# Kernel optimization log

Measured on AMD Instinct MI355X. Metric: run time of the kernel, lower is better.

The kernel has to match this reference:

```python
import jax, jax.numpy as jnp
import numpy as np

G = 8192          # graphs in batch
A = 5             # num_agents (nodes per graph)
N = G * A         # total nodes
IN_CH = 29
HID = 64
HEADS = 8
D = HID * HEADS   # 512, node/graph feature dim
NOPT = 4
ADIM = 3


def _lin(key, fan_in, fan_out):
    return jax.random.normal(key, (fan_in, fan_out), jnp.float32) / np.sqrt(fan_in)


def setup_inputs() -> dict:
    key = jax.random.key(0)
    ks = jax.random.split(key, 40)
    # --- graph structure: G fully-connected 5-node graphs + self loops ---
    pairs = np.array([(i, j) for i in range(A) for j in range(A) if i != j])  # [20,2]
    base = (np.arange(G)[:, None] * A)
    src = (base + pairs[None, :, 0]).reshape(-1)
    dst = (base + pairs[None, :, 1]).reshape(-1)
    # GATConv adds self loops (fill_value=0.0 for edge_attr)
    loop = np.arange(N)
    edge_src = jnp.asarray(np.concatenate([src, loop]), jnp.int32)
    edge_dst = jnp.asarray(np.concatenate([dst, loop]), jnp.int32)
    e_real = jax.random.uniform(ks[0], (src.shape[0], 1), jnp.float32)
    edge_attr = jnp.concatenate([e_real, jnp.zeros((N, 1), jnp.float32)], axis=0)
    batch_map = jnp.asarray(np.repeat(np.arange(G), A), jnp.int32)
    x = jax.random.normal(ks[1], (N, IN_CH), jnp.float32)
    sc = 1.0 / np.sqrt(HID)
    inp = dict(
        x=x, edge_attr=edge_attr, edge_src=edge_src, edge_dst=edge_dst, batch_map=batch_map,
        # conv1
        W1=_lin(ks[2], IN_CH, D), as1=jax.random.normal(ks[3], (HEADS, HID)) * sc,
        ad1=jax.random.normal(ks[4], (HEADS, HID)) * sc, We1=_lin(ks[5], 1, D),
        ae1=jax.random.normal(ks[6], (HEADS, HID)) * sc, b1=jnp.zeros((D,), jnp.float32),
        # conv2
        W2=_lin(ks[7], D, D), as2=jax.random.normal(ks[8], (HEADS, HID)) * sc,
        ad2=jax.random.normal(ks[9], (HEADS, HID)) * sc, We2=_lin(ks[10], 1, D),
        ae2=jax.random.normal(ks[11], (HEADS, HID)) * sc, b2=jnp.zeros((D,), jnp.float32),
        # policy-over-options head
        pw1=_lin(ks[12], D, 2 * HID), pb1=jnp.zeros((2 * HID,)), pw2=_lin(ks[13], 2 * HID, NOPT), pb2=jnp.zeros((NOPT,)),
        # q-options head
        qw1=_lin(ks[14], D, 2 * HID), qb1=jnp.zeros((2 * HID,)), qw2=_lin(ks[15], 2 * HID, NOPT), qb2=jnp.zeros((NOPT,)),
        # intra-option actor head (option 0), input dim = node + graph feature = 2*D
        aw1=_lin(ks[16], 2 * D, 2 * HID), ab1=jnp.zeros((2 * HID,)), aw2=_lin(ks[17], 2 * HID, 2 * ADIM), ab2=jnp.zeros((2 * ADIM,)),
        # termination head (option 0)
        tw1=_lin(ks[18], D, HID), tb1=jnp.zeros((HID,)), tw2=_lin(ks[19], HID, 1), tb2=jnp.zeros((1,)),
        action_limits=jnp.array([1.0, 1.0, 3.14159], jnp.float32),
    )
    return inp


def _gat(x, src, dst, eattr, W, a_s, a_d, We, a_e, b):
    n = x.shape[0]
    h = (x @ W).reshape(n, HEADS, HID)                      # [N,H,C]
    e = (eattr @ We).reshape(-1, HEADS, HID)                # [E,H,C]
    lg = ((h * a_s).sum(-1)[src] + (h * a_d).sum(-1)[dst]
          + (e * a_e).sum(-1))                              # [E,H]
    lg = jnp.where(lg > 0, lg, 0.2 * lg)                    # leaky_relu(0.2)
    m = jax.ops.segment_max(lg, dst, num_segments=n)
    p = jnp.exp(lg - m[dst])
    denom = jax.ops.segment_sum(p, dst, num_segments=n)[dst] + 1e-16
    alpha = p / denom                                       # scatter-softmax over dst
    out = jax.ops.segment_sum(alpha[:, :, None] * h[src], dst, num_segments=n)
    return out.reshape(n, HEADS * HID) + b


def reference(x, edge_attr, edge_src, edge_dst, batch_map,
              W1, as1, ad1, We1, ae1, b1,
              W2, as2, ad2, We2, ae2, b2,
              pw1, pb1, pw2, pb2, qw1, qb1, qw2, qb2,
              aw1, ab1, aw2, ab2, tw1, tb1, tw2, tb2, action_limits):
    h = jax.nn.relu(_gat(x, edge_src, edge_dst, edge_attr, W1, as1, ad1, We1, ae1, b1))
    h = jax.nn.relu(_gat(h, edge_src, edge_dst, edge_attr, W2, as2, ad2, We2, ae2, b2))
    # global_mean_pool
    cnt = jax.ops.segment_sum(jnp.ones((h.shape[0],), h.dtype), batch_map, num_segments=G)
    g = jax.ops.segment_sum(h, batch_map, num_segments=G) / cnt[:, None]   # [G,D]
    pi = jax.nn.relu(g @ pw1 + pb1) @ pw2 + pb2                            # [G,NOPT]
    q = jax.nn.relu(g @ qw1 + qb1) @ qw2 + qb2                             # [G,NOPT]
    term = jax.nn.sigmoid(jax.nn.relu(g @ tw1 + tb1) @ tw2 + tb2)          # [G,1]
    # per-graph first num_agents nodes == all nodes here (5 per graph)
    agent = h.reshape(G, A, D)
    comb = jnp.concatenate([agent, jnp.broadcast_to(g[:, None, :], (G, A, D))], axis=-1)
    ho = jax.nn.relu(comb @ aw1 + ab1) @ aw2 + ab2                          # [G,A,6]
    mean_raw, log_std_raw = jnp.split(ho, 2, axis=-1)
    mean = jnp.tanh(mean_raw) * action_limits                               # [G,A,3]
    std = 0.05 + jax.nn.sigmoid(log_std_raw) * 0.45 + 1e-6
    return jnp.concatenate([pi, q, term, mean.reshape(G, -1), std.reshape(G, -1)], axis=1)
```

## Files before the change

### kernel.cpp

```cpp
#include <hip/hip_runtime.h>
#include <hip/hip_bf16.h>
#include <math.h>

#define GG 8192
#define AA 5
#define NN (GG * AA)
#define DD 512

typedef unsigned short ushort_t;
typedef unsigned int uint_t;

__device__ inline float bf2f(ushort_t u) {
  union { uint_t i; float f; } c; c.i = ((uint_t)u) << 16; return c.f;
}
__device__ inline ushort_t f2bf(float f) {
  union { float f; uint_t i; } c; c.f = f;
  uint_t r = c.i + 0x7fffu + ((c.i >> 16) & 1u);
  return (ushort_t)(r >> 16);
}

using frag8 = __attribute__((ext_vector_type(8))) short;
using f32x4 = __attribute__((ext_vector_type(4))) float;

typedef __attribute__((address_space(3))) void lds_void;
typedef __attribute__((address_space(1))) const void gbl_void;
#define GLL(g, l) __builtin_amdgcn_global_load_lds((gbl_void*)(g), (lds_void*)(l), 16, 0, 0)

__device__ inline int xcd_swz(int bid, int nwg) {
  return (bid & 7) * (nwg >> 3) + (bid >> 3);
}

__global__ __launch_bounds__(256) void k_prep(
    const float* __restrict__ x, const float* __restrict__ W1,
    const float* __restrict__ W2, const float* __restrict__ pw1,
    const float* __restrict__ qw1, const float* __restrict__ tw1,
    const float* __restrict__ aw1, const float* __restrict__ pb1,
    const float* __restrict__ qb1, const float* __restrict__ tb1,
    const float* __restrict__ ab1, const float* __restrict__ We1,
    const float* __restrict__ ae1, const float* __restrict__ We2,
    const float* __restrict__ ae2, const float* __restrict__ as1,
    const float* __restrict__ ad1, const float* __restrict__ as2,
    const float* __restrict__ ad2, const float* __restrict__ pw2,
    const float* __restrict__ pb2, const float* __restrict__ qw2,
    const float* __restrict__ qb2, const float* __restrict__ tw2,
    const float* __restrict__ tb2, const float* __restrict__ aw2,
    const float* __restrict__ ab2, ushort_t* __restrict__ xpad32,
    ushort_t* __restrict__ W1T32, ushort_t* __restrict__ W2T,
    ushort_t* __restrict__ WcatT, ushort_t* __restrict__ aw1topT,
    ushort_t* __restrict__ wsc1T, ushort_t* __restrict__ wsc2T,
    float* __restrict__ bcat, float* __restrict__ sce,
    float* __restrict__ woutT, float* __restrict__ bout) {
  int b = blockIdx.x;
  int t = threadIdx.x;
  if (b < 1024) {
    int i = b * 256 + t;
    int n = i >> 9, k = i & 511;
    W2T[(size_t)n * 512 + k] = f2bf(W2[(size_t)k * 512 + n]);
    float v;
    if (n < 128)      v = pw1[(size_t)k * 128 + n];
    else if (n < 256) v = qw1[(size_t)k * 128 + (n - 128)];
    else if (n < 320) v = tw1[(size_t)k * 64 + (n - 256)];
    else if (n < 448) v = aw1[(size_t)(512 + k) * 128 + (n - 320)];
    else              v = 0.f;
    WcatT[(size_t)n * 512 + k] = f2bf(v);
    if (n < 128) aw1topT[(size_t)n * 512 + k] = f2bf(aw1[(size_t)k * 128 + n]);
    if (k == 0) {
      float bv;
      if (n < 128)      bv = pb1[n];
      else if (n < 256) bv = qb1[n - 128];
      else if (n < 320) bv = tb1[n - 256];
      else if (n < 448) bv = ab1[n - 320];
      else              bv = 0.f;
      bcat[n] = bv;
    }
    if (i < 512 * 32) {
      int nn = i >> 5, kk = i & 31;
      W1T32[i] = (kk < 29) ? f2bf(W1[(size_t)kk * 512 + nn]) : (ushort_t)0;
    }
    if (i < 8192) {
      int k2 = i & 511, s = i >> 9;
      int head = s >> 1;
      const float* av = ((s & 1) ? ad2 : as2) + head * 64;
      const float* wr = W2 + (size_t)k2 * 512 + head * 64;
      float val = 0.f;
      for (int c = 0; c < 64; ++c) val = fmaf(wr[c], av[c], val);
      wsc2T[i] = f2bf(val);
    }
    if (i < 512) {
      int k1 = i & 31, s = i >> 5;
      int head = s >> 1;
      float val = 0.f;
      if (k1 < 29) {
        const float* av = ((s & 1) ? ad1 : as1) + head * 64;
        const float* wr = W1 + (size_t)k1 * 512 + head * 64;
        for (int c = 0; c < 64; ++c) val = fmaf(wr[c], av[c], val);
      }
      wsc1T[i] = f2bf(val);
    }
    if (i < 16) {
      int h = i & 7;
      const float* Wp = (i < 8) ? We1 : We2;
      const float* ap = (i < 8) ? ae1 : ae2;
      float c = 0.f;
      for (int k2 = 0; k2 < 64; ++k2) c = fmaf(Wp[h * 64 + k2], ap[h * 64 + k2], c);
      sce[i] = c;
    }
    if (i < 5120) {
      int j = i / 40, o = i % 40;
      float wv;
      if (o < 4)       wv = pw2[j * 4 + o];
      else if (o < 8)  wv = qw2[j * 4 + (o - 4)];
      else if (o == 8) wv = (j < 64) ? tw2[j] : 0.f;
      else if (o < 24) wv = aw2[j * 6 + (o - 9) % 3];
      else if (o < 39) wv = aw2[j * 6 + 3 + (o - 24) % 3];
      else             wv = 0.f;
      woutT[i] = wv;
      if (j == 0) {
        float bv;
        if (o < 4)       bv = pb2[o];
        else if (o < 8)  bv = qb2[o - 4];
        else if (o == 8) bv = tb2[0];
        else if (o < 24) bv = ab2[(o - 9) % 3];
        else if (o < 39) bv = ab2[3 + (o - 24) % 3];
        else             bv = 0.f;
        bout[o] = bv;
      }
    }
  } else {
    int i = (b - 1024) * 256 + t;
    int n = i >> 5, k = i & 31;
    xpad32[i] = (k < 29) ? f2bf(x[(size_t)n * 29 + k]) : (ushort_t)0;
  }
}

__global__ __launch_bounds__(1024) void k_mega(
    const ushort_t* __restrict__ xpad32, const ushort_t* __restrict__ W1T32,
    const ushort_t* __restrict__ wsc1T, const ushort_t* __restrict__ W2T,
    const ushort_t* __restrict__ wsc2T, const float* __restrict__ eattr,
    const float* __restrict__ sce, const float* __restrict__ b1,
    const float* __restrict__ b2, ushort_t* __restrict__ h2,
    ushort_t* __restrict__ gmean) {
  __shared__ __align__(16) char smem[149504];
  const int t = threadIdx.x;
  const int lane = t & 63;
  const int w = t >> 6;
  const int l15 = lane & 15;
  const int ko2 = ((((lane >> 4) ^ (lane & 3) ^ ((lane >> 2) & 3)) & 3) * 16);
  int lid = xcd_swz(blockIdx.x, gridDim.x);
  const int m0 = lid * 80;
  const int g0 = lid * 16;
  ushort_t* h1buf = (ushort_t*)smem;
  float* sal = (float*)(smem + 124160);
  float* sss = (float*)(smem + 136960);
  float* ssd = (float*)(smem + 139520);
  const f32x4 zz = {0.f, 0.f, 0.f, 0.f};
  f32x4 acc[5][2], asc[5];
#pragma unroll
  for (int mt = 0; mt < 5; ++mt) { acc[mt][0] = zz; acc[mt][1] = zz; asc[mt] = zz; }

  {
#pragma unroll
    for (int r_ = 0; r_ < 2; ++r_) {
      int c_ = t + r_ * 1024; int row_ = c_ >> 2;
      int sw_ = ((((c_ & 3) ^ (row_ & 3) ^ ((row_ >> 2) & 3)) & 3)) * 8;
      GLL(W1T32 + (size_t)row_ * 32 + sw_, smem + 81920 + c_ * 16);
    }
    if (t < 320) {
      int c_ = t; int row_ = c_ >> 2;
      int sw_ = ((((c_ & 3) ^ (row_ & 3) ^ ((row_ >> 2) & 3)) & 3)) * 8;
      GLL(xpad32 + (size_t)(m0 + row_) * 32 + sw_, smem + 114688 + c_ * 16);
    } else if (t < 384) {
      int c_ = t - 320; int row_ = c_ >> 2;
      int sw_ = ((((c_ & 3) ^ (row_ & 3) ^ ((row_ >> 2) & 3)) & 3)) * 8;
      GLL(wsc1T + (size_t)row_ * 32 + sw_, smem + 119808 + c_ * 16);
    }
  }
  asm volatile("s_waitcnt vmcnt(0)" ::: "memory");
  __builtin_amdgcn_s_barrier();
  {
    const char* bb = smem + 81920;
    const char* aa = smem + 114688;
    const char* sb = smem + 119808;
    frag8 af[5], bfr[2];
#pragma unroll
    for (int mt = 0; mt < 5; ++mt)
      af[mt] = *(const frag8*)(aa + (mt * 16 + l15) * 64 + ko2);
#pragma unroll
    for (int n = 0; n < 2; ++n)
      bfr[n] = *(const frag8*)(bb + ((2 * w + n) * 16 + l15) * 64 + ko2);
#pragma unroll
    for (int mt = 0; mt < 5; ++mt)
#pragma unroll
      for (int n = 0; n < 2; ++n)
        acc[mt][n] = __builtin_amdgcn_mfma_f32_16x16x32_bf16(af[mt], bfr[n], acc[mt][n], 0, 0, 0);
    if (w == 15) {
      frag8 sfr = *(const frag8*)(sb + l15 * 64 + ko2);
#pragma unroll
      for (int mt = 0; mt < 5; ++mt)
        asc[mt] = __builtin_amdgcn_mfma_f32_16x16x32_bf16(af[mt], sfr, asc[mt], 0, 0, 0);
    }
  }
  if (w == 15) {
    float* dst = (l15 & 1) ? ssd : sss;
    int hd = l15 >> 1;
    int q4 = (lane >> 4) * 4;
#pragma unroll
    for (int mt = 0; mt < 5; ++mt)
#pragma unroll
      for (int r = 0; r < 4; ++r)
        dst[(mt * 16 + q4 + r) * 8 + hd] = asc[mt][r];
  }
  __syncthreads();
  if (t < 640) {
    int gi = t / 40, jh = t % 40;
    int j = jh >> 3, hd = jh & 7;
    int g = g0 + gi;
    float sdj = ssd[(gi * 5 + j) * 8 + hd];
    float ce = sce[hd];
    float lg[5], mx = -1e30f;
#pragma unroll
    for (int i = 0; i < 5; ++i) {
      float l = sss[(gi * 5 + i) * 8 + hd] + sdj;
      if (i != j) l = fmaf(eattr[(size_t)g * 20 + i * 4 + (j > i ? j - 1 : j)], ce, l);
      l = l > 0.f ? l : 0.2f * l;
      lg[i] = l; mx = fmaxf(mx, l);
    }
    float s = 0.f;
#pragma unroll
    for (int i = 0; i < 5; ++i) { lg[i] = __expf(lg[i] - mx); s += lg[i]; }
    float inv = 1.f / (s + 1e-16f);
#pragma unroll
    for (int i = 0; i < 5; ++i) sal[((gi * 5 + j) * 5 + i) * 8 + hd] = lg[i] * inv;
  }
  __syncthreads();
  {
    float* hbf = (float*)(smem + 81920);
#pragma unroll
    for (int p = 0; p < 4; ++p) {
      if ((w >> 2) == p) {
        int q4 = (lane >> 4) * 4;
#pragma unroll
        for (int mt = 0; mt < 5; ++mt)
#pragma unroll
          for (int n = 0; n < 2; ++n) {
            int lc = (w & 3) * 32 + n * 16 + l15;
#pragma unroll
            for (int r = 0; r < 4; ++r)
              hbf[(mt * 16 + q4 + r) * 132 + lc] = acc[mt][n][r];
          }
      }
      __syncthreads();
      if (t < 512) {
        int gi = t >> 5, cq = t & 31;
        int hd = 2 * p + (cq >> 4);
        int cg = p * 128 + cq * 4;
        float hv[5][4];
#pragma unroll
        for (int i = 0; i < 5; ++i)
          *(float4*)hv[i] = *(const float4*)&hbf[(gi * 5 + i) * 132 + cq * 4];
        float4 bb4 = *(const float4*)&b1[cg];
        int chunk = cg >> 5, slot = (cg >> 3) & 3, boff = (cg & 7) * 2;
#pragma unroll
        for (int j = 0; j < 5; ++j) {
          float o0 = bb4.x, o1 = bb4.y, o2 = bb4.z, o3 = bb4.w;
#pragma unroll
          for (int i = 0; i < 5; ++i) {
            float a = sal[((gi * 5 + j) * 5 + i) * 8 + hd];
            o0 = fmaf(a, hv[i][0], o0); o1 = fmaf(a, hv[i][1], o1);
            o2 = fmaf(a, hv[i][2], o2); o3 = fmaf(a, hv[i][3], o3);
          }
          o0 = fmaxf(o0, 0.f); o1 = fmaxf(o1, 0.f);
          o2 = fmaxf(o2, 0.f); o3 = fmaxf(o3, 0.f);
          uint2 wv_;
          wv_.x = (uint_t)f2bf(o0) | ((uint_t)f2bf(o1) << 16);
          wv_.y = (uint_t)f2bf(o2) | ((uint_t)f2bf(o3) << 16);
          int row = gi * 5 + j;
          int phys = slot ^ (row & 3) ^ ((row >> 2) & 3);
          *(uint2*)((char*)h1buf + chunk * 5120 + row * 64 + phys * 16 + boff) = wv_;
        }
      }
      __syncthreads();
    }
  }

#pragma unroll
  for (int mt = 0; mt < 5; ++mt) { acc[mt][0] = zz; acc[mt][1] = zz; asc[mt] = zz; }
#define FS2(bi, kk0)                                                           \
  {                                                                            \
    char* bb_ = smem + 81920 + (bi) * 32768;                                   \
    char* sb_ = smem + 147456 + (bi) * 1024;                                   \
    _Pragma("unroll")                                                          \
    for (int r_ = 0; r_ < 2; ++r_) {                                           \
      int c_ = t + r_ * 1024; int row_ = c_ >> 2;                              \
      int sw_ = ((((c_ & 3) ^ (row_ & 3) ^ ((row_ >> 2) & 3)) & 3)) * 8;       \
      GLL(W2T + (size_t)row_ * 512 + (kk0) + sw_, bb_ + c_ * 16);              \
    }                                                                          \
    if (t < 64) {                                                              \
      int c_ = t; int row_ = c_ >> 2;                                          \
      int sw_ = ((((c_ & 3) ^ (row_ & 3) ^ ((row_ >> 2) & 3)) & 3)) * 8;       \
      GLL(wsc2T + (size_t)row_ * 512 + (kk0) + sw_, sb_ + c_ * 16);            \
    }                                                                          \
  }
  FS2(0, 0);
  asm volatile("s_waitcnt vmcnt(0)" ::: "memory");
  __builtin_amdgcn_s_barrier();
  for (int ts = 0; ts < 16; ++ts) {
    int cur = ts & 1;
    if (ts + 1 < 16) FS2(cur ^ 1, (ts + 1) * 32);
    const char* bb = smem + 81920 + cur * 32768;
    const char* aa = (const char*)h1buf + ts * 5120;
    const char* sb = smem + 147456 + cur * 1024;
    frag8 af[5], bfr[2];
#pragma unroll
    for (int mt = 0; mt < 5; ++mt)
      af[mt] = *(const frag8*)(aa + (mt * 16 + l15) * 64 + ko2);
#pragma unroll
    for (int n = 0; n < 2; ++n)
      bfr[n] = *(const frag8*)(bb + ((2 * w + n) * 16 + l15) * 64 + ko2);
    __builtin_amdgcn_s_setprio(1);
#pragma unroll
    for (int mt = 0; mt < 5; ++mt)
#pragma unroll
      for (int n = 0; n < 2; ++n)
        acc[mt][n] = __builtin_amdgcn_mfma_f32_16x16x32_bf16(af[mt], bfr[n], acc[mt][n], 0, 0, 0);
    if (w == 15) {
      frag8 sfr = *(const frag8*)(sb + l15 * 64 + ko2);
#pragma unroll
      for (int mt = 0; mt < 5; ++mt)
        asc[mt] = __builtin_amdgcn_mfma_f32_16x16x32_bf16(af[mt], sfr, asc[mt], 0, 0, 0);
    }
    __builtin_amdgcn_s_setprio(0);
    __builtin_amdgcn_sched_barrier(0);
    asm volatile("s_waitcnt vmcnt(0)" ::: "memory");
    __builtin_amdgcn_s_barrier();
  }
#undef FS2
  if (w == 15) {
    float* dst = (l15 & 1) ? ssd : sss;
    int hd = l15 >> 1;
    int q4 = (lane >> 4) * 4;
#pragma unroll
    for (int mt = 0; mt < 5; ++mt)
#pragma unroll
      for (int r = 0; r < 4; ++r)
        dst[(mt * 16 + q4 + r) * 8 + hd] = asc[mt][r];
  }
  __syncthreads();
  if (t < 640) {
    int gi = t / 40, jh = t % 40;
    int j = jh >> 3, hd = jh & 7;
    int g = g0 + gi;
    float sdj = ssd[(gi * 5 + j) * 8 + hd];
    float ce = sce[8 + hd];
    float lg[5], mx = -1e30f;
#pragma unroll
    for (int i = 0; i < 5; ++i) {
      float l = sss[(gi * 5 + i) * 8 + hd] + sdj;
      if (i != j) l = fmaf(eattr[(size_t)g * 20 + i * 4 + (j > i ? j - 1 : j)], ce, l);
      l = l > 0.f ? l : 0.2f * l;
      lg[i] = l; mx = fmaxf(mx, l);
    }
    float s = 0.f;
#pragma unroll
    for (int i = 0; i < 5; ++i) { lg[i] = __expf(lg[i] - mx); s += lg[i]; }
    float inv = 1.f / (s + 1e-16f);
#pragma unroll
    for (int i = 0; i < 5; ++i) sal[((gi * 5 + j) * 5 + i) * 8 + hd] = lg[i] * inv;
  }
  __syncthreads();
  {
    float* hbf = (float*)(smem + 81920);
#pragma unroll
    for (int p = 0; p < 4; ++p) {
      if ((w >> 2) == p) {
        int q4 = (lane >> 4) * 4;
#pragma unroll
        for (int mt = 0; mt < 5; ++mt)
#pragma unroll
          for (int n = 0; n < 2; ++n) {
            int lc = (w & 3) * 32 + n * 16 + l15;
#pragma unroll
            for (int r = 0; r < 4; ++r)
              hbf[(mt * 16 + q4 + r) * 132 + lc] = acc[mt][n][r];
          }
      }
      __syncthreads();
      if (t < 512) {
        int gi = t >> 5, cq = t & 31;
        int hd = 2 * p + (cq >> 4);
        int cg = p * 128 + cq * 4;
        float hv[5][4];
#pragma unroll
        for (int i = 0; i < 5; ++i)
          *(float4*)hv[i] = *(const float4*)&hbf[(gi * 5 + i) * 132 + cq * 4];
        float4 bb4 = *(const float4*)&b2[cg];
        float gs0 = 0.f, gs1 = 0.f, gs2 = 0.f, gs3 = 0.f;
#pragma unroll
        for (int j = 0; j < 5; ++j) {
          float o0 = bb4.x, o1 = bb4.y, o2 = bb4.z, o3 = bb4.w;
#pragma unroll
          for (int i = 0; i < 5; ++i) {
            float a = sal[((gi * 5 + j) * 5 + i) * 8 + hd];
            o0 = fmaf(a, hv[i][0], o0); o1 = fmaf(a, hv[i][1], o1);
            o2 = fmaf(a, hv[i][2], o2); o3 = fmaf(a, hv[i][3], o3);
          }
          o0 = fmaxf(o0, 0.f); o1 = fmaxf(o1, 0.f);
          o2 = fmaxf(o2, 0.f); o3 = fmaxf(o3, 0.f);
          uint2 wv_;
          wv_.x = (uint_t)f2bf(o0) | ((uint_t)f2bf(o1) << 16);
          wv_.y = (uint_t)f2bf(o2) | ((uint_t)f2bf(o3) << 16);
          *(uint2*)(h2 + ((size_t)(g0 + gi) * 5 + j) * 512 + cg) = wv_;
          gs0 += o0; gs1 += o1; gs2 += o2; gs3 += o3;
        }
        uint2 wv_;
        wv_.x = (uint_t)f2bf(gs0 * 0.2f) | ((uint_t)f2bf(gs1 * 0.2f) << 16);
        wv_.y = (uint_t)f2bf(gs2 * 0.2f) | ((uint_t)f2bf(gs3 * 0.2f) << 16);
        *(uint2*)(gmean + (size_t)(g0 + gi) * 512 + cg) = wv_;
      }
      __syncthreads();
    }
  }
}

template <int EPI>
__device__ __forceinline__ void gemm_body(
    const ushort_t* __restrict__ A, const ushort_t* __restrict__ BT,
    const float* __restrict__ bias, void* __restrict__ Cv,
    int M, int N, int K, int m0, int n0, char* lds) {
  int t = threadIdx.x;
  int lane = t & 63;
  int wv = t >> 6;
  int wr = (wv >> 1) * 64, wc = (wv & 1) * 64;
  f32x4 acc[4][4] = {};
  int ch0 = t, ch1 = t + 256;
  int row0 = ch0 >> 2, row1 = ch1 >> 2;
  int sw0 = (((ch0 & 3) ^ (row0 & 3) ^ ((row0 >> 2) & 3)) & 3) * 8;
  int sw1 = (((ch1 & 3) ^ (row1 & 3) ^ ((row1 >> 2) & 3)) & 3) * 8;
  int ko2 = ((((lane >> 4) ^ (lane & 3) ^ ((lane >> 2) & 3)) & 3) * 16);
  const int nt = K >> 5;
#define STAGE(bi, kk0)                                                         \
  {                                                                            \
    char* ab = lds + (bi) * 16384;                                             \
    GLL(A + (size_t)(m0 + row0) * K + (kk0) + sw0, ab + ch0 * 16);             \
    GLL(A + (size_t)(m0 + row1) * K + (kk0) + sw1, ab + ch1 * 16);             \
    GLL(BT + (size_t)(n0 + row0) * K + (kk0) + sw0, ab + 8192 + ch0 * 16);     \
    GLL(BT + (size_t)(n0 + row1) * K + (kk0) + sw1, ab + 8192 + ch1 * 16);     \
  }
  STAGE(0, 0);
  if (nt > 1) STAGE(1, 32);
  for (int ts = 0; ts < nt; ++ts) {
    int bi = ts % 3;
    if (ts + 2 < nt) {
      STAGE((ts + 2) % 3, (ts + 2) * 32);
      asm volatile("s_waitcnt vmcnt(8)" ::: "memory");
    } else if (ts + 1 < nt) {
      asm volatile("s_waitcnt vmcnt(4)" ::: "memory");
    } else {
      asm volatile("s_waitcnt vmcnt(0)" ::: "memory");
    }
    __builtin_amdgcn_s_barrier();
    __builtin_amdgcn_sched_barrier(0);
    const char* ab = lds + bi * 16384;
    frag8 af[4], bfr[4];
#pragma unroll
    for (int m = 0; m < 4; ++m)
      af[m] = *(const frag8*)(ab + (wr + m * 16 + (lane & 15)) * 64 + ko2);
#pragma unroll
    for (int n = 0; n < 4; ++n)
      bfr[n] = *(const frag8*)(ab + 8192 + (wc + n * 16 + (lane & 15)) * 64 + ko2);
#pragma unroll
    for (int m = 0; m < 4; ++m)
#pragma unroll
      for (int n = 0; n < 4; ++n)
        acc[m][n] = __builtin_amdgcn_mfma_f32_16x16x32_bf16(af[m], bfr[n], acc[m][n], 0, 0, 0);
    __builtin_amdgcn_sched_barrier(0);
    __builtin_amdgcn_s_barrier();
  }
#undef STAGE
  int r4 = (lane >> 4) * 4;
  int cl = lane & 15;
#pragma unroll
  for (int m = 0; m < 4; ++m) {
#pragma unroll
    for (int n = 0; n < 4; ++n) {
      int col = n0 + wc + n * 16 + cl;
      float bb = (EPI == 2) ? bias[col] : 0.f;
#pragma unroll
      for (int r = 0; r < 4; ++r) {
        int row = m0 + wr + m * 16 + r4 + r;
        float v = acc[m][n][r] + bb;
        if (EPI == 2 && col < 320) v = fmaxf(v, 0.f);
        ((float*)Cv)[(size_t)row * N + col] = v;
      }
    }
  }
}

__global__ __launch_bounds__(256) void k_hgemm(
    const ushort_t* __restrict__ h2, const ushort_t* __restrict__ aw1topT,
    float* __restrict__ ahid, const ushort_t* __restrict__ gmean,
    const ushort_t* __restrict__ WcatT, const float* __restrict__ bcat,
    float* __restrict__ hcat) {
  __shared__ char lds[49152];
  int bid = blockIdx.x;
  if (bid < 320) {
    int lid = xcd_swz(bid, 320);
    gemm_body<1>(h2, aw1topT, nullptr, ahid, NN, 128, DD, lid * 128, 0, lds);
  } else {
    int lid = xcd_swz(bid - 320, 256);
    gemm_body<2>(gmean, WcatT, bcat, hcat, GG, DD, DD, (lid >> 2) * 128, (lid & 3) * 128, lds);
  }
}

__global__ __launch_bounds__(256) void k_heads(
    const float* __restrict__ hcat, const float* __restrict__ ahid,
    const float* __restrict__ woutT, const float* __restrict__ bout,
    const float* __restrict__ alim, float* __restrict__ out) {
  int g0 = blockIdx.x * 4;
  int t = threadIdx.x;
  __shared__ float sbuf[4224];
  for (int i = t; i < 4224; i += 256) {
    int gi = i / 1056, r = i - gi * 1056;
    const float* grow = hcat + (size_t)(g0 + gi) * 512;
    float v = 0.f;
    if (r < 128)                  v = grow[r];
    else if (r >= 132 && r < 260) v = grow[128 + r - 132];
    else if (r >= 264 && r < 328) v = grow[256 + r - 264];
    else if (r >= 396) {
      int q = r - 396; int a = q / 132; int j = q - a * 132;
      if (j < 128)
        v = fmaxf(ahid[((size_t)(g0 + gi) * 5 + a) * 128 + j] + grow[320 + j], 0.f);
    }
    sbuf[i] = v;
  }
  __syncthreads();
  int gi = t >> 6, o = t & 63;
  int oc = o < 39 ? o : 39;
  int seg;
  if (oc < 4)       seg = 0;
  else if (oc < 8)  seg = 132;
  else if (oc == 8) seg = 264;
  else {
    int idx = (oc < 24) ? oc - 9 : oc - 24;
    seg = 396 + (idx / 3) * 132;
  }
  const float* ip = &sbuf[gi * 1056 + seg];
  float a0 = 0.f, a1 = 0.f, a2 = 0.f, a3 = 0.f;
#pragma unroll
  for (int j = 0; j < 128; j += 4) {
    a0 = fmaf(ip[j + 0], woutT[(j + 0) * 40 + oc], a0);
    a1 = fmaf(ip[j + 1], woutT[(j + 1) * 40 + oc], a1);
    a2 = fmaf(ip[j + 2], woutT[(j + 2) * 40 + oc], a2);
    a3 = fmaf(ip[j + 3], woutT[(j + 3) * 40 + oc], a3);
  }
  float res = (a0 + a1) + (a2 + a3) + bout[oc];
  if (o < 39) {
    if (o == 8)       res = 1.f / (1.f + __expf(-res));
    else if (o >= 24) res = 0.05f + 0.45f / (1.f + __expf(-res)) + 1e-6f;
    else if (o >= 9)  res = tanhf(res) * alim[(o - 9) % 3];
    out[(size_t)(g0 + gi) * 39 + o] = res;
  }
}

extern "C" void kernel_launch(void* const* d_in, const int* in_sizes, int n_in,
                              void* d_out, int out_size, void* d_ws, size_t ws_size,
                              hipStream_t stream) {
  const float* x     = (const float*)d_in[0];
  const float* eattr = (const float*)d_in[1];
  const float* W1  = (const float*)d_in[5];
  const float* as1 = (const float*)d_in[6];
  const float* ad1 = (const float*)d_in[7];
  const float* We1 = (const float*)d_in[8];
  const float* ae1 = (const float*)d_in[9];
  const float* b1  = (const float*)d_in[10];
  const float* W2  = (const float*)d_in[11];
  const float* as2 = (const float*)d_in[12];
  const float* ad2 = (const float*)d_in[13];
  const float* We2 = (const float*)d_in[14];
  const float* ae2 = (const float*)d_in[15];
  const float* b2  = (const float*)d_in[16];
  const float* pw1 = (const float*)d_in[17];
  const float* pb1 = (const float*)d_in[18];
  const float* pw2 = (const float*)d_in[19];
  const float* pb2 = (const float*)d_in[20];
  const float* qw1 = (const float*)d_in[21];
  const float* qb1 = (const float*)d_in[22];
  const float* qw2 = (const float*)d_in[23];
  const float* qb2 = (const float*)d_in[24];
  const float* aw1 = (const float*)d_in[25];
  const float* ab1 = (const float*)d_in[26];
  const float* aw2 = (const float*)d_in[27];
  const float* ab2 = (const float*)d_in[28];
  const float* tw1 = (const float*)d_in[29];
  const float* tb1 = (const float*)d_in[30];
  const float* tw2 = (const float*)d_in[31];
  const float* tb2 = (const float*)d_in[32];
  const float* alim = (const float*)d_in[33];

  const size_t BIGE = (size_t)NN * DD;
  char* p = (char*)d_ws;
  ushort_t* h2     = (ushort_t*)p; p += BIGE * 2;
  ushort_t* gmean  = (ushort_t*)p; p += (size_t)GG * DD * 2;
  ushort_t* xpad32 = (ushort_t*)p; p += (size_t)NN * 32 * 2;
  ushort_t* W1T32  = (ushort_t*)p; p += (size_t)512 * 32 * 2;
  ushort_t* W2T    = (ushort_t*)p; p += (size_t)512 * 512 * 2;
  ushort_t* WcatT  = (ushort_t*)p; p += (size_t)512 * 512 * 2;
  ushort_t* aw1topT = (ushort_t*)p; p += (size_t)128 * 512 * 2;
  ushort_t* wsc1T  = (ushort_t*)p; p += (size_t)16 * 32 * 2;
  ushort_t* wsc2T  = (ushort_t*)p; p += (size_t)16 * 512 * 2;
  float* bcat  = (float*)p; p += 512 * 4;
  float* sce   = (float*)p; p += 16 * 4;
  float* woutT = (float*)p; p += 5120 * 4;
  float* bout  = (float*)p; p += 40 * 4;
  float* ahid  = (float*)p; p += (size_t)NN * 128 * 4;
  float* hcat  = (float*)p;

  k_prep<<<1024 + 5120, 256, 0, stream>>>(
      x, W1, W2, pw1, qw1, tw1, aw1, pb1, qb1, tb1, ab1,
      We1, ae1, We2, ae2, as1, ad1, as2, ad2,
      pw2, pb2, qw2, qb2, tw2, tb2, aw2, ab2,
      xpad32, W1T32, W2T, WcatT, aw1topT, wsc1T, wsc2T,
      bcat, sce, woutT, bout);
  k_mega<<<GG / 16, 1024, 0, stream>>>(
      xpad32, W1T32, wsc1T, W2T, wsc2T, eattr, sce, b1, b2, h2, gmean);
  k_hgemm<<<320 + 256, 256, 0, stream>>>(h2, aw1topT, ahid, gmean, WcatT, bcat, hcat);
  k_heads<<<GG / 4, 256, 0, stream>>>(hcat, ahid, woutT, bout, alim, (float*)d_out);
}
```

Before: 110.0 us.

## Store head GEMM intermediates in bf16 and switch to double-buffered pipeline

The intermediate outputs ahid and hcat are now written as bf16 instead of fp32, which halves their store and reload traffic between the head GEMM and the heads kernel. The GEMM K-loop moves from a 3-stage to a 2-stage LDS pipeline, with a full vmcnt(0) wait each iteration and s_setprio raised around the MFMA block. LDS use drops from 48KB to 32KB, which may allow more resident blocks. The costs are lower precision in the intermediates and less latency hiding on global loads.

```diff
diff --git a/kernel.cpp b/kernel.cpp
--- a/kernel.cpp
+++ b/kernel.cpp
@@ -425,7 +425,7 @@
 template <int EPI>
 __device__ __forceinline__ void gemm_body(
     const ushort_t* __restrict__ A, const ushort_t* __restrict__ BT,
-    const float* __restrict__ bias, void* __restrict__ Cv,
+    const float* __restrict__ bias, ushort_t* __restrict__ Cv,
     int M, int N, int K, int m0, int n0, char* lds) {
   int t = threadIdx.x;
   int lane = t & 63;
@@ -447,20 +447,12 @@
     GLL(BT + (size_t)(n0 + row1) * K + (kk0) + sw1, ab + 8192 + ch1 * 16);     \
   }
   STAGE(0, 0);
-  if (nt > 1) STAGE(1, 32);
+  asm volatile("s_waitcnt vmcnt(0)" ::: "memory");
+  __builtin_amdgcn_s_barrier();
   for (int ts = 0; ts < nt; ++ts) {
-    int bi = ts % 3;
-    if (ts + 2 < nt) {
-      STAGE((ts + 2) % 3, (ts + 2) * 32);
-      asm volatile("s_waitcnt vmcnt(8)" ::: "memory");
-    } else if (ts + 1 < nt) {
-      asm volatile("s_waitcnt vmcnt(4)" ::: "memory");
-    } else {
-      asm volatile("s_waitcnt vmcnt(0)" ::: "memory");
-    }
-    __builtin_amdgcn_s_barrier();
-    __builtin_amdgcn_sched_barrier(0);
-    const char* ab = lds + bi * 16384;
+    int cur = ts & 1;
+    if (ts + 1 < nt) STAGE(cur ^ 1, (ts + 1) * 32);
+    const char* ab = lds + cur * 16384;
     frag8 af[4], bfr[4];
 #pragma unroll
     for (int m = 0; m < 4; ++m)
@@ -468,12 +460,15 @@
 #pragma unroll
     for (int n = 0; n < 4; ++n)
       bfr[n] = *(const frag8*)(ab + 8192 + (wc + n * 16 + (lane & 15)) * 64 + ko2);
+    __builtin_amdgcn_s_setprio(1);
 #pragma unroll
     for (int m = 0; m < 4; ++m)
 #pragma unroll
       for (int n = 0; n < 4; ++n)
         acc[m][n] = __builtin_amdgcn_mfma_f32_16x16x32_bf16(af[m], bfr[n], acc[m][n], 0, 0, 0);
+    __builtin_amdgcn_s_setprio(0);
     __builtin_amdgcn_sched_barrier(0);
+    asm volatile("s_waitcnt vmcnt(0)" ::: "memory");
     __builtin_amdgcn_s_barrier();
   }
 #undef STAGE
@@ -490,7 +485,7 @@
         int row = m0 + wr + m * 16 + r4 + r;
         float v = acc[m][n][r] + bb;
         if (EPI == 2 && col < 320) v = fmaxf(v, 0.f);
-        ((float*)Cv)[(size_t)row * N + col] = v;
+        Cv[(size_t)row * N + col] = f2bf(v);
       }
     }
   }
@@ -498,10 +493,10 @@
 
 __global__ __launch_bounds__(256) void k_hgemm(
     const ushort_t* __restrict__ h2, const ushort_t* __restrict__ aw1topT,
-    float* __restrict__ ahid, const ushort_t* __restrict__ gmean,
+    ushort_t* __restrict__ ahid, const ushort_t* __restrict__ gmean,
     const ushort_t* __restrict__ WcatT, const float* __restrict__ bcat,
-    float* __restrict__ hcat) {
-  __shared__ char lds[49152];
+    ushort_t* __restrict__ hcat) {
+  __shared__ char lds[32768];
   int bid = blockIdx.x;
   if (bid < 320) {
     int lid = xcd_swz(bid, 320);
@@ -513,7 +508,7 @@
 }
 
 __global__ __launch_bounds__(256) void k_heads(
-    const float* __restrict__ hcat, const float* __restrict__ ahid,
+    const ushort_t* __restrict__ hcat, const ushort_t* __restrict__ ahid,
     const float* __restrict__ woutT, const float* __restrict__ bout,
     const float* __restrict__ alim, float* __restrict__ out) {
   int g0 = blockIdx.x * 4;
@@ -521,15 +516,15 @@
   __shared__ float sbuf[4224];
   for (int i = t; i < 4224; i += 256) {
     int gi = i / 1056, r = i - gi * 1056;
-    const float* grow = hcat + (size_t)(g0 + gi) * 512;
+    const ushort_t* grow = hcat + (size_t)(g0 + gi) * 512;
     float v = 0.f;
-    if (r < 128)                  v = grow[r];
-    else if (r >= 132 && r < 260) v = grow[128 + r - 132];
-    else if (r >= 264 && r < 328) v = grow[256 + r - 264];
+    if (r < 128)                  v = bf2f(grow[r]);
+    else if (r >= 132 && r < 260) v = bf2f(grow[128 + r - 132]);
+    else if (r >= 264 && r < 328) v = bf2f(grow[256 + r - 264]);
     else if (r >= 396) {
       int q = r - 396; int a = q / 132; int j = q - a * 132;
       if (j < 128)
-        v = fmaxf(ahid[((size_t)(g0 + gi) * 5 + a) * 128 + j] + grow[320 + j], 0.f);
+        v = fmaxf(bf2f(ahid[((size_t)(g0 + gi) * 5 + a) * 128 + j]) + bf2f(grow[320 + j]), 0.f);
     }
     sbuf[i] = v;
   }
@@ -612,8 +607,8 @@
   float* sce   = (float*)p; p += 16 * 4;
   float* woutT = (float*)p; p += 5120 * 4;
   float* bout  = (float*)p; p += 40 * 4;
-  float* ahid  = (float*)p; p += (size_t)NN * 128 * 4;
-  float* hcat  = (float*)p;
+  ushort_t* ahid = (ushort_t*)p; p += (size_t)NN * 128 * 2;
+  ushort_t* hcat = (ushort_t*)p;
 
   k_prep<<<1024 + 5120, 256, 0, stream>>>(
       x, W1, W2, pw1, qw1, tw1, aw1, pb1, qb1, tb1, ab1,
```

Result: faster. 105.8 us, median of 2 (-3.9%).
